# Performance work log

Hardware: AMD Instinct MI355X
Metric: run time of the kernel (lower is better)

## Reference

```python
import jax, jax.numpy as jnp
import numpy as np

B, N = 8192, 64
EPS = 1e-3  # diagonal jitter to guarantee strict positive-definiteness


def setup_inputs() -> dict:
    key = jax.random.key(0)
    A = jax.random.normal(key, (B, N, N), dtype=jnp.float32)
    # SPD construction: X = A A^T / N + eps*I  (eigenvalues strictly > 0)
    X = jnp.einsum('bik,bjk->bij', A, A) / N + EPS * jnp.eye(N, dtype=jnp.float32)
    return {"X": X}


def reference(X):
    # sym_logm: eig-based matrix logarithm of batched SPD matrices
    w, v = jnp.linalg.eigh(X)                    # w: [B,N], v: [B,N,N]
    logm = jnp.einsum('bik,bk,bjk->bij', v, jnp.log(w), v)  # V diag(log w) V^T
    # embed with tril=False: flatten from dim 1 -> [B, N*N]
    return logm.reshape(logm.shape[0], -1)
```

## Files before the change

kernel.cpp:

```cpp
#include <hip/hip_runtime.h>
#include <math.h>

#define NSW 12

__device__ __forceinline__ float bperm_f(int addr4, float v) {
    return __int_as_float(__builtin_amdgcn_ds_bpermute(addr4, __float_as_int(v)));
}

__global__ __launch_bounds__(128, 4) void logeig_kernel(
    const float* __restrict__ Xg, float* __restrict__ out)
{
    __shared__ __align__(16) float Wc[64 * 20];
    __shared__ float gbuf[2][2][64];
    __shared__ float nbuf[2][64];
    __shared__ float hlds[64];

    const int tid = threadIdx.x;
    const int w   = tid >> 6;
    const int l   = tid & 63;
    const int b   = blockIdx.x;

    float x[32];
    {
        const float4* __restrict__ Xb4 =
            (const float4*)(Xg + (size_t)b * 4096 + (size_t)l * 64 + 32 * w);
        #pragma unroll
        for (int q = 0; q < 8; ++q) {
            float4 v = Xb4[q];
            x[4 * q + 0] = v.x; x[4 * q + 1] = v.y;
            x[4 * q + 2] = v.z; x[4 * q + 3] = v.w;
        }
    }

    float d;
    {
        float a0 = 0.f, a1 = 0.f, a2 = 0.f, a3 = 0.f;
        #pragma unroll
        for (int k = 0; k < 32; k += 4) {
            a0 = fmaf(x[k + 0], x[k + 0], a0);
            a1 = fmaf(x[k + 1], x[k + 1], a1);
            a2 = fmaf(x[k + 2], x[k + 2], a2);
            a3 = fmaf(x[k + 3], x[k + 3], a3);
        }
        nbuf[w][l] = (a0 + a1) + (a2 + a3);
        __syncthreads();
        d = nbuf[0][l] + nbuf[1][l];
    }

    const int m  = l - 1;
    int pm = (l == 0) ? 0 : ((63 - m) % 63);
    int p0 = 0;

    for (int sweep = 0; sweep < NSW; ++sweep) {
        for (int r = 0; r < 63; ++r) {
            const int prt  = (l == 0) ? (p0 + 1)
                                      : ((pm == m) ? 0 : (pm + 1));
            const int prt4 = prt << 2;

            float xp[32];
            float g0 = 0.f, g1 = 0.f, g2 = 0.f, g3 = 0.f;
            #pragma unroll
            for (int k = 0; k < 32; k += 4) {
                xp[k + 0] = bperm_f(prt4, x[k + 0]);
                xp[k + 1] = bperm_f(prt4, x[k + 1]);
                xp[k + 2] = bperm_f(prt4, x[k + 2]);
                xp[k + 3] = bperm_f(prt4, x[k + 3]);
                g0 = fmaf(x[k + 0], xp[k + 0], g0);
                g1 = fmaf(x[k + 1], xp[k + 1], g1);
                g2 = fmaf(x[k + 2], xp[k + 2], g2);
                g3 = fmaf(x[k + 3], xp[k + 3], g3);
            }
            const float gp = (g0 + g1) + (g2 + g3);
            const float dq = bperm_f(prt4, d);

            gbuf[r & 1][w][l] = gp;
            __syncthreads();
            const float go = gbuf[r & 1][1 - w][l];
            const float g  = gp + go;

            const bool lo = l < prt;
            const bool ok = fabsf(g) > 1e-30f;

            const float num  = lo ? (dq - d) : (d - dq);
            const float zeta = num / (2.f * g);
            const float az   = fabsf(zeta);
            float tl = 1.f / (az + sqrtf(fmaf(az, az, 1.f)));
            tl = (zeta >= 0.f) ? tl : -tl;
            float tn = lo ? tl : -tl;
            tn = ok ? tn : 0.f;
            const float c = rsqrtf(fmaf(tn, tn, 1.f));
            const float s = c * tn;

            d = fmaf(-tn, g, d);

            #pragma unroll
            for (int k = 0; k < 32; ++k)
                x[k] = fmaf(-s, xp[k], c * x[k]);

            pm = (pm + 1 == 63) ? 0 : (pm + 1);
            p0 += 32; if (p0 >= 63) p0 -= 63;
        }

        float a0 = 0.f, a1 = 0.f, a2 = 0.f, a3 = 0.f;
        #pragma unroll
        for (int k = 0; k < 32; k += 4) {
            a0 = fmaf(x[k + 0], x[k + 0], a0);
            a1 = fmaf(x[k + 1], x[k + 1], a1);
            a2 = fmaf(x[k + 2], x[k + 2], a2);
            a3 = fmaf(x[k + 3], x[k + 3], a3);
        }
        __syncthreads();
        nbuf[w][l] = (a0 + a1) + (a2 + a3);
        __syncthreads();
        d = nbuf[0][l] + nbuf[1][l];
    }

    const float alpha = fmaxf(d, 1e-12f);
    const float h = 0.5f * logf(alpha) / alpha;
    if (w == 0) hlds[l] = h;

    float acc[32];
    #pragma unroll
    for (int j = 0; j < 32; ++j) acc[j] = 0.f;

    const int cg = l >> 4;
    const int cc = l & 15;

    for (int gi = 0; gi < 4; ++gi) {
        __syncthreads();
        if (cg == gi) {
            #pragma unroll
            for (int j = 0; j < 32; ++j) Wc[(32 * w + j) * 20 + cc] = x[j];
        }
        __syncthreads();

        float r0[16];
        #pragma unroll
        for (int jj = 0; jj < 16; ++jj) r0[jj] = Wc[l * 20 + jj] * hlds[gi * 16 + jj];

        #pragma unroll
        for (int j = 0; j < 32; ++j) {
            const int row = 32 * w + j;
            const float4 wa = *(const float4*)&Wc[row * 20 + 0];
            const float4 wb = *(const float4*)&Wc[row * 20 + 4];
            const float4 wv = *(const float4*)&Wc[row * 20 + 8];
            const float4 wd = *(const float4*)&Wc[row * 20 + 12];
            float t0 = fmaf(wa.x, r0[0],  fmaf(wa.y, r0[1],  fmaf(wa.z, r0[2],  wa.w * r0[3])));
            float t1 = fmaf(wb.x, r0[4],  fmaf(wb.y, r0[5],  fmaf(wb.z, r0[6],  wb.w * r0[7])));
            float t2 = fmaf(wv.x, r0[8],  fmaf(wv.y, r0[9],  fmaf(wv.z, r0[10], wv.w * r0[11])));
            float t3 = fmaf(wd.x, r0[12], fmaf(wd.y, r0[13], fmaf(wd.z, r0[14], wd.w * r0[15])));
            acc[j] += (t0 + t1) + (t2 + t3);
        }
    }

    float* __restrict__ outb = out + (size_t)b * 4096;
    #pragma unroll
    for (int j = 0; j < 32; ++j)
        outb[(size_t)(32 * w + j) * 64 + l] = acc[j];
}

extern "C" void kernel_launch(void* const* d_in, const int* in_sizes, int n_in,
                              void* d_out, int out_size, void* d_ws, size_t ws_size,
                              hipStream_t stream)
{
    const float* X = (const float*)d_in[0];
    float* out = (float*)d_out;
    const int B = in_sizes[0] / 4096;
    logeig_kernel<<<dim3(B), dim3(128), 0, stream>>>(X, out);
}
```

Before: 5.123 ms.

## Split each Jacobi matrix across four wavefronts instead of two

Each block now uses 256 threads (four wavefronts), and each wavefront holds 16 columns of a row instead of 32. This halves per-thread registers and the serial bpermute/FMA chain per rotation, so more wavefronts can run per matrix and the per-round latency should drop. In exchange, every round's partial dot products need a four-way LDS reduction at the block barrier, and four waves now synchronize per rotation instead of two. Total wavefront count and occupancy pressure per CU also rise.

Result: slower. 6.295 ms (+22.9%).

```diff
diff --git a/kernel.cpp b/kernel.cpp
--- a/kernel.cpp
+++ b/kernel.cpp
@@ -7,12 +7,11 @@
     return __int_as_float(__builtin_amdgcn_ds_bpermute(addr4, __float_as_int(v)));
 }
 
-__global__ __launch_bounds__(128, 4) void logeig_kernel(
+__global__ __launch_bounds__(256, 4) void logeig_kernel(
     const float* __restrict__ Xg, float* __restrict__ out)
 {
     __shared__ __align__(16) float Wc[64 * 20];
-    __shared__ float gbuf[2][2][64];
-    __shared__ float nbuf[2][64];
+    __shared__ float gbuf[2][4][64];
     __shared__ float hlds[64];
 
     const int tid = threadIdx.x;
@@ -20,31 +19,39 @@
     const int l   = tid & 63;
     const int b   = blockIdx.x;
 
-    float x[32];
+    float x[16];
     {
         const float4* __restrict__ Xb4 =
-            (const float4*)(Xg + (size_t)b * 4096 + (size_t)l * 64 + 32 * w);
+            (const float4*)(Xg + (size_t)b * 4096 + (size_t)l * 64 + 16 * w);
         #pragma unroll
-        for (int q = 0; q < 8; ++q) {
+        for (int q = 0; q < 4; ++q) {
             float4 v = Xb4[q];
             x[4 * q + 0] = v.x; x[4 * q + 1] = v.y;
             x[4 * q + 2] = v.z; x[4 * q + 3] = v.w;
         }
     }
 
+    #define SELFDOT16(res)                                            \
+        {                                                             \
+            float a0 = 0.f, a1 = 0.f, a2 = 0.f, a3 = 0.f;             \
+            _Pragma("unroll")                                         \
+            for (int k = 0; k < 16; k += 4) {                         \
+                a0 = fmaf(x[k + 0], x[k + 0], a0);                    \
+                a1 = fmaf(x[k + 1], x[k + 1], a1);                    \
+                a2 = fmaf(x[k + 2], x[k + 2], a2);                    \
+                a3 = fmaf(x[k + 3], x[k + 3], a3);                    \
+            }                                                         \
+            res = (a0 + a1) + (a2 + a3);                              \
+        }
+
     float d;
     {
-        float a0 = 0.f, a1 = 0.f, a2 = 0.f, a3 = 0.f;
-        #pragma unroll
-        for (int k = 0; k < 32; k += 4) {
-            a0 = fmaf(x[k + 0], x[k + 0], a0);
-            a1 = fmaf(x[k + 1], x[k + 1], a1);
-            a2 = fmaf(x[k + 2], x[k + 2], a2);
-            a3 = fmaf(x[k + 3], x[k + 3], a3);
-        }
-        nbuf[w][l] = (a0 + a1) + (a2 + a3);
+        float p; SELFDOT16(p);
+        gbuf[0][w][l] = p;
         __syncthreads();
-        d = nbuf[0][l] + nbuf[1][l];
+        const float g0 = gbuf[0][0][l], g1 = gbuf[0][1][l];
+        const float g2 = gbuf[0][2][l], g3 = gbuf[0][3][l];
+        d = (g0 + g1) + (g2 + g3);
     }
 
     const int m  = l - 1;
@@ -57,26 +64,27 @@
                                       : ((pm == m) ? 0 : (pm + 1));
             const int prt4 = prt << 2;
 
-            float xp[32];
-            float g0 = 0.f, g1 = 0.f, g2 = 0.f, g3 = 0.f;
+            float xp[16];
+            float a0 = 0.f, a1 = 0.f, a2 = 0.f, a3 = 0.f;
             #pragma unroll
-            for (int k = 0; k < 32; k += 4) {
+            for (int k = 0; k < 16; k += 4) {
                 xp[k + 0] = bperm_f(prt4, x[k + 0]);
                 xp[k + 1] = bperm_f(prt4, x[k + 1]);
                 xp[k + 2] = bperm_f(prt4, x[k + 2]);
                 xp[k + 3] = bperm_f(prt4, x[k + 3]);
-                g0 = fmaf(x[k + 0], xp[k + 0], g0);
-                g1 = fmaf(x[k + 1], xp[k + 1], g1);
-                g2 = fmaf(x[k + 2], xp[k + 2], g2);
-                g3 = fmaf(x[k + 3], xp[k + 3], g3);
+                a0 = fmaf(x[k + 0], xp[k + 0], a0);
+                a1 = fmaf(x[k + 1], xp[k + 1], a1);
+                a2 = fmaf(x[k + 2], xp[k + 2], a2);
+                a3 = fmaf(x[k + 3], xp[k + 3], a3);
             }
-            const float gp = (g0 + g1) + (g2 + g3);
+            const float gp = (a0 + a1) + (a2 + a3);
             const float dq = bperm_f(prt4, d);
 
             gbuf[r & 1][w][l] = gp;
             __syncthreads();
-            const float go = gbuf[r & 1][1 - w][l];
-            const float g  = gp + go;
+            const float g0 = gbuf[r & 1][0][l], g1 = gbuf[r & 1][1][l];
+            const float g2 = gbuf[r & 1][2][l], g3 = gbuf[r & 1][3][l];
+            const float g  = (g0 + g1) + (g2 + g3);
 
             const bool lo = l < prt;
             const bool ok = fabsf(g) > 1e-30f;
@@ -94,34 +102,30 @@
             d = fmaf(-tn, g, d);
 
             #pragma unroll
-            for (int k = 0; k < 32; ++k)
+            for (int k = 0; k < 16; ++k)
                 x[k] = fmaf(-s, xp[k], c * x[k]);
 
             pm = (pm + 1 == 63) ? 0 : (pm + 1);
             p0 += 32; if (p0 >= 63) p0 -= 63;
         }
 
-        float a0 = 0.f, a1 = 0.f, a2 = 0.f, a3 = 0.f;
-        #pragma unroll
-        for (int k = 0; k < 32; k += 4) {
-            a0 = fmaf(x[k + 0], x[k + 0], a0);
-            a1 = fmaf(x[k + 1], x[k + 1], a1);
-            a2 = fmaf(x[k + 2], x[k + 2], a2);
-            a3 = fmaf(x[k + 3], x[k + 3], a3);
-        }
+        float p; SELFDOT16(p);
         __syncthreads();
-        nbuf[w][l] = (a0 + a1) + (a2 + a3);
+        gbuf[0][w][l] = p;
         __syncthreads();
-        d = nbuf[0][l] + nbuf[1][l];
+        const float g0 = gbuf[0][0][l], g1 = gbuf[0][1][l];
+        const float g2 = gbuf[0][2][l], g3 = gbuf[0][3][l];
+        d = (g0 + g1) + (g2 + g3);
     }
+    #undef SELFDOT16
 
     const float alpha = fmaxf(d, 1e-12f);
     const float h = 0.5f * logf(alpha) / alpha;
     if (w == 0) hlds[l] = h;
 
-    float acc[32];
+    float acc[16];
     #pragma unroll
-    for (int j = 0; j < 32; ++j) acc[j] = 0.f;
+    for (int k = 0; k < 16; ++k) acc[k] = 0.f;
 
     const int cg = l >> 4;
     const int cc = l & 15;
@@ -130,17 +134,17 @@
         __syncthreads();
         if (cg == gi) {
             #pragma unroll
-            for (int j = 0; j < 32; ++j) Wc[(32 * w + j) * 20 + cc] = x[j];
+            for (int k = 0; k < 16; ++k) Wc[(16 * w + k) * 20 + cc] = x[k];
         }
         __syncthreads();
 
         float r0[16];
         #pragma unroll
-        for (int jj = 0; jj < 16; ++jj) r0[jj] = Wc[l * 20 + jj] * hlds[gi * 16 + jj];
+        for (int j = 0; j < 16; ++j) r0[j] = Wc[l * 20 + j] * hlds[gi * 16 + j];
 
         #pragma unroll
-        for (int j = 0; j < 32; ++j) {
-            const int row = 32 * w + j;
+        for (int k = 0; k < 16; ++k) {
+            const int row = 16 * w + k;
             const float4 wa = *(const float4*)&Wc[row * 20 + 0];
             const float4 wb = *(const float4*)&Wc[row * 20 + 4];
             const float4 wv = *(const float4*)&Wc[row * 20 + 8];
@@ -149,14 +153,14 @@
             float t1 = fmaf(wb.x, r0[4],  fmaf(wb.y, r0[5],  fmaf(wb.z, r0[6],  wb.w * r0[7])));
             float t2 = fmaf(wv.x, r0[8],  fmaf(wv.y, r0[9],  fmaf(wv.z, r0[10], wv.w * r0[11])));
             float t3 = fmaf(wd.x, r0[12], fmaf(wd.y, r0[13], fmaf(wd.z, r0[14], wd.w * r0[15])));
-            acc[j] += (t0 + t1) + (t2 + t3);
+            acc[k] += (t0 + t1) + (t2 + t3);
         }
     }
 
     float* __restrict__ outb = out + (size_t)b * 4096;
     #pragma unroll
-    for (int j = 0; j < 32; ++j)
-        outb[(size_t)(32 * w + j) * 64 + l] = acc[j];
+    for (int k = 0; k < 16; ++k)
+        outb[(size_t)(16 * w + k) * 64 + l] = acc[k];
 }
 
 extern "C" void kernel_launch(void* const* d_in, const int* in_sizes, int n_in,
@@ -166,5 +170,5 @@
     const float* X = (const float*)d_in[0];
     float* out = (float*)d_out;
     const int B = in_sizes[0] / 4096;
-    logeig_kernel<<<dim3(B), dim3(128), 0, stream>>>(X, out);
+    logeig_kernel<<<dim3(B), dim3(256), 0, stream>>>(X, out);
 }
```
